# Kernel tuning notes

Measured on AMD Instinct MI355X. Metric: run time of the kernel, lower is better.

The kernel has to match this reference:

```python
import jax, jax.numpy as jnp
import numpy as np

B, T, H, DI, DO = 512, 512, 100, 101, 2
DT_OVER_TAU = 0.1  # dt=1, tau=10


def retanh(x):
    return jnp.maximum(jnp.tanh(x), 0.0)


def setup_inputs() -> dict:
    key = jax.random.key(0)
    k0, k1, k2, k3 = jax.random.split(key, 4)
    inp = jax.random.normal(k0, (B, T, DI), jnp.float32)
    noise = jax.random.normal(k1, (B, T, H), jnp.float32) * 0.1
    W_x_ah = (jax.random.normal(k2, (H, DI), jnp.float32) / np.sqrt(DI)).astype(jnp.float32)
    b_ah = jnp.zeros((H,), jnp.float32)
    # orthogonalized recurrent weights (svd with unit singular values), as in __init__
    A = np.random.default_rng(0).standard_normal((H, H))
    u, _, vT = np.linalg.svd(A)
    W_h_ah = jnp.asarray(u @ vT, jnp.float32)
    # original inits W_h_y to zeros; use small random so output is nontrivial
    W_h_y = jax.random.normal(k3, (DO, H), jnp.float32) * 0.1
    ah0 = jnp.zeros((H,), jnp.float32)
    return {"input": inp, "noise": noise, "W_x_ah": W_x_ah, "b_ah": b_ah,
            "W_h_ah": W_h_ah, "W_h_y": W_h_y, "ah0": ah0}


def reference(input, noise, W_x_ah, b_ah, W_h_ah, W_h_y, ah0):
    # precompute input projection as one batched GEMM: [B,T,H]
    xp = jnp.einsum('bti,hi->bth', input, W_x_ah) + b_ah
    ah_init = jnp.broadcast_to(ah0, (input.shape[0], ah0.shape[0]))
    h_init = retanh(ah_init)

    def step(carry, xs):
        ah, h = carry
        xp_t, nz_t = xs
        ah = ah + DT_OVER_TAU * (-ah + h @ W_h_ah.T + xp_t)
        h = retanh(ah) + nz_t
        return (ah, h), h

    _, hstore = jax.lax.scan(step, (ah_init, h_init),
                             (xp.transpose(1, 0, 2), noise.transpose(1, 0, 2)))
    hstore = hstore.transpose(1, 0, 2)  # [B,T,H]
    output = hstore @ W_h_y.T  # [B,T,DO]
    return output, hstore
```

## Files before the change

kernel.cpp:

```cpp
#include <hip/hip_runtime.h>
#include <hip/hip_bf16.h>

#define BB 512
#define TT 512
#define HH 100
#define DI 101
#define DOUT 2
#define BT (BB * TT)

__global__ __launch_bounds__(128, 2) void k_inproj(
    const float* __restrict__ in, const float* __restrict__ Wx,
    const float* __restrict__ bias, float* __restrict__ xp) {
  const int t = threadIdx.x;
  const int p = t >> 1;
  const int kh = t & 1;
  const int c0 = p;
  const int c1 = p + 64;
  const bool c1ok = (c1 < HH);

  __shared__ __align__(16) float Atile[64 * 104];

  float4 wx0[13], wx1[13];
  {
    const float* w0 = Wx + (size_t)c0 * DI + kh * 52;
    const float* w1 = Wx + (size_t)(c1ok ? c1 : 0) * DI + kh * 52;
    const int nk = kh ? 49 : 52;
#pragma unroll
    for (int j = 0; j < 13; ++j) {
      float a0 = (4 * j + 0 < nk) ? w0[4 * j + 0] : 0.f;
      float a1 = (4 * j + 1 < nk) ? w0[4 * j + 1] : 0.f;
      float a2 = (4 * j + 2 < nk) ? w0[4 * j + 2] : 0.f;
      float a3 = (4 * j + 3 < nk) ? w0[4 * j + 3] : 0.f;
      wx0[j] = make_float4(a0, a1, a2, a3);
      float b0v = (4 * j + 0 < nk) ? w1[4 * j + 0] : 0.f;
      float b1v = (4 * j + 1 < nk) ? w1[4 * j + 1] : 0.f;
      float b2v = (4 * j + 2 < nk) ? w1[4 * j + 2] : 0.f;
      float b3v = (4 * j + 3 < nk) ? w1[4 * j + 3] : 0.f;
      wx1[j] = make_float4(b0v, b1v, b2v, b3v);
    }
  }
  const float bs0 = bias[c0];
  const float bs1 = c1ok ? bias[c1] : 0.f;

  const int row0 = blockIdx.x * 64;

  {
    const float* rp = in + (size_t)(row0 + p) * DI + kh * 52;
    float* dst = Atile + p * 104 + kh * 52;
#pragma unroll
    for (int j = 0; j < 52; ++j) {
      float v;
      if (kh == 0) v = rp[j];
      else        v = (52 + j < DI) ? rp[j] : 0.f;
      dst[j] = v;
    }
  }
  __syncthreads();

#pragma unroll 2
  for (int r = 0; r < 64; ++r) {
    const float4* a4 = (const float4*)(Atile + r * 104 + kh * 52);
    float4 s0 = make_float4(0.f, 0.f, 0.f, 0.f);
    float4 s1 = make_float4(0.f, 0.f, 0.f, 0.f);
#pragma unroll
    for (int j = 0; j < 13; ++j) {
      float4 av = a4[j];
      s0.x = fmaf(av.x, wx0[j].x, s0.x);
      s0.y = fmaf(av.y, wx0[j].y, s0.y);
      s0.z = fmaf(av.z, wx0[j].z, s0.z);
      s0.w = fmaf(av.w, wx0[j].w, s0.w);
      s1.x = fmaf(av.x, wx1[j].x, s1.x);
      s1.y = fmaf(av.y, wx1[j].y, s1.y);
      s1.z = fmaf(av.z, wx1[j].z, s1.z);
      s1.w = fmaf(av.w, wx1[j].w, s1.w);
    }
    float p0 = (s0.x + s0.y) + (s0.z + s0.w);
    float p1 = (s1.x + s1.y) + (s1.z + s1.w);
    p0 += __shfl_xor(p0, 1, 64);
    p1 += __shfl_xor(p1, 1, 64);
    if (kh == 0) {
      float* xr = xp + (size_t)(row0 + r) * HH;
      xr[c0] = p0 + bs0;
      if (c1ok) xr[c1] = p1 + bs1;
    }
  }
}

__global__ __launch_bounds__(256, 2) void k_scan(
    const float* __restrict__ noise, const float* __restrict__ Wh,
    const float* __restrict__ ah0, float* hstore ) {
  const int b = blockIdx.x;
  const int t = threadIdx.x;
  const int w = t >> 6;
  const int l = t & 63;
  const int i = (w << 5) + (l >> 1);
  const int kh = l & 1;
  const bool act = (i < HH);
  const int ie = act ? i : 0;
  const int hb = kh * 13;

  __shared__ __align__(16) float h_lds[2][104];

  float4 wh4[13];
  {
    const float4* wr = (const float4*)(Wh + (size_t)ie * HH + kh * 52);
#pragma unroll
    for (int j = 0; j < 13; ++j) {
      if (j < 12 || kh == 0) wh4[j] = wr[j];
      else wh4[j] = make_float4(0.f, 0.f, 0.f, 0.f);
    }
  }

  float ah = ah0[ie];
  {
    float e = __expf(-2.f * ah);
    float h0 = (ah > 0.f) ? (1.f - e) * __builtin_amdgcn_rcpf(1.f + e) : 0.f;
    if (act && kh == 0) h_lds[0][i] = h0;
  }
  if (t < 8) h_lds[t >> 2][100 + (t & 3)] = 0.f;
  __syncthreads();

  const float* xp_base = hstore;
  const size_t bbase = (size_t)b * TT * HH;

  float xpA = xp_base[bbase + 0 * HH + ie];
  float nzA = noise[bbase + 0 * HH + ie];
  float xpB = xp_base[bbase + 1 * HH + ie];
  float nzB = noise[bbase + 1 * HH + ie];
  float xpC = xp_base[bbase + 2 * HH + ie];
  float nzC = noise[bbase + 2 * HH + ie];
  float xpD = xp_base[bbase + 3 * HH + ie];
  float nzD = noise[bbase + 3 * HH + ie];

#define STEP(XP, NZ, tc)                                                     \
  {                                                                          \
    const int tpf = (tc) + 4;                                                \
    float nxp = 0.f, nnz = 0.f;                                              \
    if (tpf < TT) {                                                          \
      nxp = xp_base[bbase + (size_t)tpf * HH + ie];                          \
      nnz = noise[bbase + (size_t)tpf * HH + ie];                            \
    }                                                                        \
    const float4* h4 = (const float4*)h_lds[(tc)&1];                         \
    float4 acc = make_float4(0.f, 0.f, 0.f, 0.f);                            \
    _Pragma("unroll") for (int j = 0; j < 13; ++j) {                         \
      float4 hv = h4[hb + j];                                                \
      acc.x = fmaf(wh4[j].x, hv.x, acc.x);                                   \
      acc.y = fmaf(wh4[j].y, hv.y, acc.y);                                   \
      acc.z = fmaf(wh4[j].z, hv.z, acc.z);                                   \
      acc.w = fmaf(wh4[j].w, hv.w, acc.w);                                   \
    }                                                                        \
    float d = (acc.x + acc.y) + (acc.z + acc.w);                             \
    d += __int_as_float(__builtin_amdgcn_mov_dpp(                            \
        __float_as_int(d), 0xB1, 0xF, 0xF, true));     \
    ah = fmaf(0.1f, (d + XP) - ah, ah);                                      \
    float e = __expf(-2.f * ah);                                             \
    float h = (ah > 0.f) ? (1.f - e) * __builtin_amdgcn_rcpf(1.f + e) : 0.f; \
    h += NZ;                                                                 \
    if (act && kh == 0) {                                                    \
      h_lds[((tc) + 1) & 1][i] = h;                                          \
      hstore[bbase + (size_t)(tc)*HH + i] = h;                               \
    }                                                                        \
    \
    asm volatile("s_waitcnt lgkmcnt(0)\n\ts_barrier" ::: "memory");          \
    XP = nxp;                                                                \
    NZ = nnz;                                                                \
  }

#pragma unroll 1
  for (int tc = 0; tc < TT; tc += 4) {
    STEP(xpA, nzA, tc);
    STEP(xpB, nzB, tc + 1);
    STEP(xpC, nzC, tc + 2);
    STEP(xpD, nzD, tc + 3);
  }
#undef STEP
}

__global__ __launch_bounds__(256, 2) void k_outproj(
    const float* __restrict__ hstore, const float* __restrict__ Wy,
    float* __restrict__ out) {
  __shared__ __align__(16) float wy_l[2][HH];
  const int t = threadIdx.x;
  if (t < 2 * HH) {
    int r = t / HH;
    int c = t - r * HH;
    wy_l[r][c] = Wy[t];
  }
  __syncthreads();

  const int row = blockIdx.x * 256 + t;
  const float4* h4 = (const float4*)(hstore + (size_t)row * HH);
  const float4* w0 = (const float4*)wy_l[0];
  const float4* w1 = (const float4*)wy_l[1];
  float4 a0 = make_float4(0.f, 0.f, 0.f, 0.f);
  float4 a1 = make_float4(0.f, 0.f, 0.f, 0.f);
#pragma unroll
  for (int j = 0; j < 25; ++j) {
    float4 hv = h4[j];
    float4 x0 = w0[j];
    float4 x1 = w1[j];
    a0.x = fmaf(hv.x, x0.x, a0.x);
    a0.y = fmaf(hv.y, x0.y, a0.y);
    a0.z = fmaf(hv.z, x0.z, a0.z);
    a0.w = fmaf(hv.w, x0.w, a0.w);
    a1.x = fmaf(hv.x, x1.x, a1.x);
    a1.y = fmaf(hv.y, x1.y, a1.y);
    a1.z = fmaf(hv.z, x1.z, a1.z);
    a1.w = fmaf(hv.w, x1.w, a1.w);
  }
  float d0 = (a0.x + a0.y) + (a0.z + a0.w);
  float d1 = (a1.x + a1.y) + (a1.z + a1.w);
  ((float2*)out)[row] = make_float2(d0, d1);
}

extern "C" void kernel_launch(void* const* d_in, const int* in_sizes, int n_in,
                              void* d_out, int out_size, void* d_ws,
                              size_t ws_size, hipStream_t stream) {
  const float* input = (const float*)d_in[0];
  const float* noise = (const float*)d_in[1];
  const float* W_x = (const float*)d_in[2];
  const float* b_ah = (const float*)d_in[3];
  const float* W_h = (const float*)d_in[4];
  const float* W_y = (const float*)d_in[5];
  const float* ah0 = (const float*)d_in[6];

  float* out = (float*)d_out;
  float* hstore = out + (size_t)BB * TT * DOUT;

  k_inproj<<<BT / 64, 128, 0, stream>>>(input, W_x, b_ah, hstore);

  k_scan<<<BB, 256, 0, stream>>>(noise, W_h, ah0, hstore);

  k_outproj<<<BT / 256, 256, 0, stream>>>(hstore, W_y, out);
}
```

Measured before the change: 627.0 us.

## Run recurrent scan in a single wavefront and fuse the output projection

The scan kernel now uses one 64-lane wavefront per batch element. Each active lane owns two hidden units and keeps both full rows of W_h in registers, so the per-step cross-wave barriers and DPP partial-sum exchange go away. The output projection is computed inside the scan with a shuffle reduction each step, which removes the separate kernel that re-read hstore. In exchange, each lane's dot-product chain is longer, register pressure is much higher, and the serial loop gains six shuffle rounds per step.

```diff
diff --git a/kernel.cpp b/kernel.cpp
--- a/kernel.cpp
+++ b/kernel.cpp
@@ -7,6 +7,8 @@
 #define DI 101
 #define DOUT 2
 #define BT (BB * TT)
+
+typedef float f4 __attribute__((ext_vector_type(4)));
 
 __global__ __launch_bounds__(128, 2) void k_inproj(
     const float* __restrict__ in, const float* __restrict__ Wx,
@@ -86,84 +88,116 @@
   }
 }
 
-__global__ __launch_bounds__(256, 2) void k_scan(
+__global__ __launch_bounds__(64, 1) void k_scan(
     const float* __restrict__ noise, const float* __restrict__ Wh,
-    const float* __restrict__ ah0, float* hstore ) {
+    const float* __restrict__ ah0, const float* __restrict__ Wy,
+    float* __restrict__ out, float* hstore ) {
   const int b = blockIdx.x;
-  const int t = threadIdx.x;
-  const int w = t >> 6;
-  const int l = t & 63;
-  const int i = (w << 5) + (l >> 1);
-  const int kh = l & 1;
-  const bool act = (i < HH);
-  const int ie = act ? i : 0;
-  const int hb = kh * 13;
-
-  __shared__ __align__(16) float h_lds[2][104];
-
-  float4 wh4[13];
-  {
-    const float4* wr = (const float4*)(Wh + (size_t)ie * HH + kh * 52);
-#pragma unroll
-    for (int j = 0; j < 13; ++j) {
-      if (j < 12 || kh == 0) wh4[j] = wr[j];
-      else wh4[j] = make_float4(0.f, 0.f, 0.f, 0.f);
-    }
-  }
-
-  float ah = ah0[ie];
-  {
-    float e = __expf(-2.f * ah);
-    float h0 = (ah > 0.f) ? (1.f - e) * __builtin_amdgcn_rcpf(1.f + e) : 0.f;
-    if (act && kh == 0) h_lds[0][i] = h0;
-  }
-  if (t < 8) h_lds[t >> 2][100 + (t & 3)] = 0.f;
-  __syncthreads();
+  const int l = threadIdx.x;
+  const bool act = (l < 50);
+  const int s0 = act ? 2 * l : 0;
+
+  __shared__ __align__(16) float h_lds[HH];
+
+  f4 w0[25], w1[25];
+  {
+    const f4* r0 = (const f4*)(Wh + (size_t)s0 * HH);
+    const f4* r1 = (const f4*)(Wh + (size_t)(s0 + 1) * HH);
+#pragma unroll
+    for (int j = 0; j < 25; ++j) {
+      w0[j] = r0[j];
+      w1[j] = r1[j];
+    }
+  }
+  float wy00 = 0.f, wy01 = 0.f, wy10 = 0.f, wy11 = 0.f;
+  if (act) {
+    float2 wa = *(const float2*)(Wy + s0);
+    float2 wb = *(const float2*)(Wy + HH + s0);
+    wy00 = wa.x; wy01 = wa.y; wy10 = wb.x; wy11 = wb.y;
+  }
+
+  float ahx = 0.f, ahy = 0.f;
+  if (act) {
+    float2 a = *(const float2*)(ah0 + s0);
+    ahx = a.x; ahy = a.y;
+  }
+  {
+    float e0 = __expf(-2.f * ahx);
+    float e1 = __expf(-2.f * ahy);
+    float h0 = (ahx > 0.f) ? (1.f - e0) * __builtin_amdgcn_rcpf(1.f + e0) : 0.f;
+    float h1 = (ahy > 0.f) ? (1.f - e1) * __builtin_amdgcn_rcpf(1.f + e1) : 0.f;
+    if (act) *(float2*)&h_lds[s0] = make_float2(h0, h1);
+  }
 
   const float* xp_base = hstore;
   const size_t bbase = (size_t)b * TT * HH;
-
-  float xpA = xp_base[bbase + 0 * HH + ie];
-  float nzA = noise[bbase + 0 * HH + ie];
-  float xpB = xp_base[bbase + 1 * HH + ie];
-  float nzB = noise[bbase + 1 * HH + ie];
-  float xpC = xp_base[bbase + 2 * HH + ie];
-  float nzC = noise[bbase + 2 * HH + ie];
-  float xpD = xp_base[bbase + 3 * HH + ie];
-  float nzD = noise[bbase + 3 * HH + ie];
-
-#define STEP(XP, NZ, tc)                                                     \
-  {                                                                          \
-    const int tpf = (tc) + 4;                                                \
-    float nxp = 0.f, nnz = 0.f;                                              \
-    if (tpf < TT) {                                                          \
-      nxp = xp_base[bbase + (size_t)tpf * HH + ie];                          \
-      nnz = noise[bbase + (size_t)tpf * HH + ie];                            \
-    }                                                                        \
-    const float4* h4 = (const float4*)h_lds[(tc)&1];                         \
-    float4 acc = make_float4(0.f, 0.f, 0.f, 0.f);                            \
-    _Pragma("unroll") for (int j = 0; j < 13; ++j) {                         \
-      float4 hv = h4[hb + j];                                                \
-      acc.x = fmaf(wh4[j].x, hv.x, acc.x);                                   \
-      acc.y = fmaf(wh4[j].y, hv.y, acc.y);                                   \
-      acc.z = fmaf(wh4[j].z, hv.z, acc.z);                                   \
-      acc.w = fmaf(wh4[j].w, hv.w, acc.w);                                   \
-    }                                                                        \
-    float d = (acc.x + acc.y) + (acc.z + acc.w);                             \
-    d += __int_as_float(__builtin_amdgcn_mov_dpp(                            \
-        __float_as_int(d), 0xB1, 0xF, 0xF, true));     \
-    ah = fmaf(0.1f, (d + XP) - ah, ah);                                      \
-    float e = __expf(-2.f * ah);                                             \
-    float h = (ah > 0.f) ? (1.f - e) * __builtin_amdgcn_rcpf(1.f + e) : 0.f; \
-    h += NZ;                                                                 \
-    if (act && kh == 0) {                                                    \
-      h_lds[((tc) + 1) & 1][i] = h;                                          \
-      hstore[bbase + (size_t)(tc)*HH + i] = h;                               \
-    }                                                                        \
-    \
-    asm volatile("s_waitcnt lgkmcnt(0)\n\ts_barrier" ::: "memory");          \
-    XP = nxp;                                                                \
-    NZ = nnz;                                                                \
+  float2* out2 = (float2*)out;
+
+  float2 xpA = make_float2(0.f, 0.f), nzA = xpA;
+  float2 xpB = xpA, nzB = xpA, xpC = xpA, nzC = xpA, xpD = xpA, nzD = xpA;
+  if (act) {
+    xpA = *(const float2*)(xp_base + bbase + (size_t)0 * HH + s0);
+    nzA = *(const float2*)(noise + bbase + (size_t)0 * HH + s0);
+    xpB = *(const float2*)(xp_base + bbase + (size_t)1 * HH + s0);
+    nzB = *(const float2*)(noise + bbase + (size_t)1 * HH + s0);
+    xpC = *(const float2*)(xp_base + bbase + (size_t)2 * HH + s0);
+    nzC = *(const float2*)(noise + bbase + (size_t)2 * HH + s0);
+    xpD = *(const float2*)(xp_base + bbase + (size_t)3 * HH + s0);
+    nzD = *(const float2*)(noise + bbase + (size_t)3 * HH + s0);
+  }
+
+#define STEP(XP, NZ, tc)                                                      \
+  {                                                                           \
+    const int tpf = (tc) + 4;                                                 \
+    float2 nxp = make_float2(0.f, 0.f), nnz = nxp;                            \
+    if (act && tpf < TT) {                                                    \
+      nxp = *(const float2*)(xp_base + bbase + (size_t)tpf * HH + s0);        \
+      nnz = *(const float2*)(noise + bbase + (size_t)tpf * HH + s0);          \
+    }                                                                         \
+    const f4* h4 = (const f4*)h_lds;                                          \
+    f4 acc0 = {0.f, 0.f, 0.f, 0.f};                                           \
+    f4 acc1 = {0.f, 0.f, 0.f, 0.f};                                           \
+    _Pragma("unroll") for (int j = 0; j < 25; ++j) {                          \
+      f4 hv = h4[j];                      \
+      acc0 = __builtin_elementwise_fma(w0[j], hv, acc0);                      \
+      acc1 = __builtin_elementwise_fma(w1[j], hv, acc1);                      \
+    }                                                                         \
+    float d0 = (acc0.x + acc0.y) + (acc0.z + acc0.w);                         \
+    float d1 = (acc1.x + acc1.y) + (acc1.z + acc1.w);                         \
+    ahx = fmaf(0.1f, (d0 + XP.x) - ahx, ahx);                                 \
+    ahy = fmaf(0.1f, (d1 + XP.y) - ahy, ahy);                                 \
+    float e0 = __expf(-2.f * ahx);                                            \
+    float e1 = __expf(-2.f * ahy);                                            \
+    float h0 = (ahx > 0.f) ? (1.f - e0) * __builtin_amdgcn_rcpf(1.f + e0)     \
+                           : 0.f;                                             \
+    float h1 = (ahy > 0.f) ? (1.f - e1) * __builtin_amdgcn_rcpf(1.f + e1)     \
+                           : 0.f;                                             \
+    h0 += NZ.x;                                                               \
+    h1 += NZ.y;                                                               \
+             \
+    if (act) {                                                                \
+      *(float2*)&h_lds[s0] = make_float2(h0, h1);                             \
+      *(float2*)(hstore + bbase + (size_t)(tc)*HH + s0) =                     \
+          make_float2(h0, h1);                                                \
+    }                                                                         \
+               \
+    float po0 = act ? fmaf(h0, wy00, h1 * wy01) : 0.f;                        \
+    float po1 = act ? fmaf(h0, wy10, h1 * wy11) : 0.f;                        \
+    po0 += __shfl_xor(po0, 1, 64);                                            \
+    po1 += __shfl_xor(po1, 1, 64);                                            \
+    po0 += __shfl_xor(po0, 2, 64);                                            \
+    po1 += __shfl_xor(po1, 2, 64);                                            \
+    po0 += __shfl_xor(po0, 4, 64);                                            \
+    po1 += __shfl_xor(po1, 4, 64);                                            \
+    po0 += __shfl_xor(po0, 8, 64);                                            \
+    po1 += __shfl_xor(po1, 8, 64);                                            \
+    po0 += __shfl_xor(po0, 16, 64);                                           \
+    po1 += __shfl_xor(po1, 16, 64);                                           \
+    po0 += __shfl_xor(po0, 32, 64);                                           \
+    po1 += __shfl_xor(po1, 32, 64);                                           \
+    if (l == 0) out2[(size_t)b * TT + (tc)] = make_float2(po0, po1);          \
+    XP = nxp;                                                                 \
+    NZ = nnz;                                                                 \
   }
 
 #pragma unroll 1
@@ -174,43 +208,6 @@
     STEP(xpD, nzD, tc + 3);
   }
 #undef STEP
-}
-
-__global__ __launch_bounds__(256, 2) void k_outproj(
-    const float* __restrict__ hstore, const float* __restrict__ Wy,
-    float* __restrict__ out) {
-  __shared__ __align__(16) float wy_l[2][HH];
-  const int t = threadIdx.x;
-  if (t < 2 * HH) {
-    int r = t / HH;
-    int c = t - r * HH;
-    wy_l[r][c] = Wy[t];
-  }
-  __syncthreads();
-
-  const int row = blockIdx.x * 256 + t;
-  const float4* h4 = (const float4*)(hstore + (size_t)row * HH);
-  const float4* w0 = (const float4*)wy_l[0];
-  const float4* w1 = (const float4*)wy_l[1];
-  float4 a0 = make_float4(0.f, 0.f, 0.f, 0.f);
-  float4 a1 = make_float4(0.f, 0.f, 0.f, 0.f);
-#pragma unroll
-  for (int j = 0; j < 25; ++j) {
-    float4 hv = h4[j];
-    float4 x0 = w0[j];
-    float4 x1 = w1[j];
-    a0.x = fmaf(hv.x, x0.x, a0.x);
-    a0.y = fmaf(hv.y, x0.y, a0.y);
-    a0.z = fmaf(hv.z, x0.z, a0.z);
-    a0.w = fmaf(hv.w, x0.w, a0.w);
-    a1.x = fmaf(hv.x, x1.x, a1.x);
-    a1.y = fmaf(hv.y, x1.y, a1.y);
-    a1.z = fmaf(hv.z, x1.z, a1.z);
-    a1.w = fmaf(hv.w, x1.w, a1.w);
-  }
-  float d0 = (a0.x + a0.y) + (a0.z + a0.w);
-  float d1 = (a1.x + a1.y) + (a1.z + a1.w);
-  ((float2*)out)[row] = make_float2(d0, d1);
 }
 
 extern "C" void kernel_launch(void* const* d_in, const int* in_sizes, int n_in,
@@ -229,7 +226,5 @@
 
   k_inproj<<<BT / 64, 128, 0, stream>>>(input, W_x, b_ah, hstore);
 
-  k_scan<<<BB, 256, 0, stream>>>(noise, W_h, ah0, hstore);
-
-  k_outproj<<<BT / 256, 256, 0, stream>>>(hstore, W_y, out);
+  k_scan<<<BB, 64, 0, stream>>>(noise, W_h, ah0, W_y, out, hstore);
 }
```

Result: slower. 727.7 us (+16.1%).
